# Performance work log

Hardware: AMD Instinct MI355X
Metric: run time of the kernel (lower is better)

Reference implementation:

```python
import jax, jax.numpy as jnp
import numpy as np

B, N, D, F = 16, 64, 32, 32  # batch, nodes, node_dim, nb_features


def setup_inputs() -> dict:
    key = jax.random.key(0)
    k1, k2, k3, k4, k5 = jax.random.split(key, 5)
    nodes = jax.random.normal(k1, (B, N, D), dtype=jnp.float32)
    edges = jax.random.normal(k2, (B, N * N, F), dtype=jnp.float32)
    mask = jax.random.randint(k3, (B, N * N, 1), 0, 2).astype(jnp.float32)
    # Linear(nb_features -> node_dim**2) params, torch-style fan-in scaling
    lim = 1.0 / np.sqrt(F)
    W = jax.random.uniform(k4, (D * D, F), dtype=jnp.float32, minval=-lim, maxval=lim)
    b = jax.random.uniform(k5, (D * D,), dtype=jnp.float32, minval=-lim, maxval=lim)
    return {"nodes": nodes, "edges": edges, "mask": mask, "W": W, "b": b}


def reference(nodes, edges, mask, W, b):
    Bn, Nn, d = nodes.shape
    # ECC weight generation: per-edge d x d matrix from edge features
    A = jax.nn.relu(jnp.einsum('bef,gf->beg', edges, W) + b)      # [B, N*N, d*d]
    A = A.reshape(Bn, Nn, Nn, d, d)                               # [B, i, j, d, d]
    # node_j tiling: flat edge index i*N+j pairs with source node j
    messages = jnp.einsum('bijde,bje->bijd', A, nodes)            # [B, i, j, d]
    masked = messages * mask.reshape(Bn, Nn, Nn, 1)
    agg_m = jnp.sum(masked, axis=2)                               # [B, N, d]
    return agg_m
```

## Files before the change

kernel.cpp:

```cpp
#include <hip/hip_runtime.h>
#include <hip/hip_bf16.h>


#define B_ 16
#define N_ 64
#define D_ 32
#define F_ 32
#define NP 33

typedef __attribute__((ext_vector_type(8))) short bf16x8;
typedef __attribute__((ext_vector_type(4))) float f32x4;

__device__ __forceinline__ short f2bf(float x) {
    unsigned u = __builtin_bit_cast(unsigned, x);
    u += 0x7fffu + ((u >> 16) & 1u);
    return (short)(u >> 16);
}

__global__ __launch_bounds__(256, 4) void ecc_fused_kernel(
    const float* __restrict__ nodes,
    const float* __restrict__ edges,
    const float* __restrict__ mask,
    const float* __restrict__ W,
    const float* __restrict__ bias,
    float* __restrict__ out)
{
    __shared__ float nmask[N_ * NP];

    const int tid  = threadIdx.x;
    const int lane = tid & 63;
    const int wv   = tid >> 6;
    const int col  = lane & 15;
    const int grp  = lane >> 4;
    const int bi   = blockIdx.x;
    const int b    = bi >> 6;
    const int i    = bi & 63;
    const int f0   = grp * 8;

    {
        const int j  = tid >> 2;
        const int c0 = (tid & 3) * 8;
        const float mk = mask[b * (N_ * N_) + i * N_ + j];
        const float* np = nodes + (b * N_ + j) * D_ + c0;
        f32x4 v0 = *(const f32x4*)np;
        f32x4 v1 = *(const f32x4*)(np + 4);
        float* dst = &nmask[j * NP + c0];
        dst[0] = v0[0] * mk; dst[1] = v0[1] * mk;
        dst[2] = v0[2] * mk; dst[3] = v0[3] * mk;
        dst[4] = v1[0] * mk; dst[5] = v1[1] * mk;
        dst[6] = v1[2] * mk; dst[7] = v1[3] * mk;
    }
    __syncthreads();

    const float* eb = edges + (b * (N_ * N_) + i * N_) * F_;
    bf16x8 bfrag[4];
#pragma unroll
    for (int jt = 0; jt < 4; ++jt) {
        const float* s = eb + (jt * 16 + col) * F_ + f0;
        f32x4 e0 = *(const f32x4*)s;
        f32x4 e1 = *(const f32x4*)(s + 4);
        bf16x8 t;
        t[0] = f2bf(e0[0]); t[1] = f2bf(e0[1]); t[2] = f2bf(e0[2]); t[3] = f2bf(e0[3]);
        t[4] = f2bf(e1[0]); t[5] = f2bf(e1[1]); t[6] = f2bf(e1[2]); t[7] = f2bf(e1[3]);
        bfrag[jt] = t;
    }

    float acc[8] = {0.f, 0.f, 0.f, 0.f, 0.f, 0.f, 0.f, 0.f};

#pragma unroll 1
    for (int par = 0; par < 2; ++par) {
        float nd[4][4];
#pragma unroll
        for (int jt = 0; jt < 4; ++jt) {
            const float* n = &nmask[(jt * 16 + col) * NP + par * 16 + grp * 4];
            nd[jt][0] = n[0]; nd[jt][1] = n[1];
            nd[jt][2] = n[2]; nd[jt][3] = n[3];
        }
#pragma unroll
        for (int g8 = 0; g8 < 8; ++g8) {
            const int gt = wv * 16 + g8 * 2 + par;
            const float* ws = W + (gt * 16 + col) * F_ + f0;
            f32x4 w0 = *(const f32x4*)ws;
            f32x4 w1 = *(const f32x4*)(ws + 4);
            bf16x8 afrag;
            afrag[0] = f2bf(w0[0]); afrag[1] = f2bf(w0[1]);
            afrag[2] = f2bf(w0[2]); afrag[3] = f2bf(w0[3]);
            afrag[4] = f2bf(w1[0]); afrag[5] = f2bf(w1[1]);
            afrag[6] = f2bf(w1[2]); afrag[7] = f2bf(w1[3]);

            f32x4 bfr = *(const f32x4*)(bias + gt * 16 + grp * 4);

#pragma unroll
            for (int jt = 0; jt < 4; ++jt) {
                f32x4 c = __builtin_amdgcn_mfma_f32_16x16x32_bf16(afrag, bfrag[jt], bfr, 0, 0, 0);
                float s = fmaxf(c[0], 0.f) * nd[jt][0];
                s += fmaxf(c[1], 0.f) * nd[jt][1];
                s += fmaxf(c[2], 0.f) * nd[jt][2];
                s += fmaxf(c[3], 0.f) * nd[jt][3];
                acc[g8] += s;
            }
        }
    }

#pragma unroll
    for (int dl = 0; dl < 8; ++dl) {
        float v = acc[dl];
#pragma unroll
        for (int off = 32; off > 0; off >>= 1) v += __shfl_xor(v, off, 64);
        acc[dl] = v;
    }

    if (lane == 0) {
        float* op = out + (b * N_ + i) * D_ + wv * 8;
#pragma unroll
        for (int dl = 0; dl < 8; ++dl) op[dl] = acc[dl];
    }
}

extern "C" void kernel_launch(void* const* d_in, const int* in_sizes, int n_in,
                              void* d_out, int out_size, void* d_ws, size_t ws_size,
                              hipStream_t stream) {
    const float* nodes = (const float*)d_in[0];
    const float* edges = (const float*)d_in[1];
    const float* mask  = (const float*)d_in[2];
    const float* W     = (const float*)d_in[3];
    const float* bias  = (const float*)d_in[4];
    float* outp        = (float*)d_out;

    ecc_fused_kernel<<<dim3(B_ * N_), dim3(256), 0, stream>>>(
        nodes, edges, mask, W, bias, outp);
}
```

Before: 105.1 us.

## Stage bf16-converted W half and bias in LDS per parity pass

```diff
diff --git a/kernel.cpp b/kernel.cpp
--- a/kernel.cpp
+++ b/kernel.cpp
@@ -17,7 +17,7 @@
     return (short)(u >> 16);
 }
 
-__global__ __launch_bounds__(256, 4) void ecc_fused_kernel(
+__global__ __launch_bounds__(256) void ecc_fused_kernel(
     const float* __restrict__ nodes,
     const float* __restrict__ edges,
     const float* __restrict__ mask,
@@ -25,7 +25,9 @@
     const float* __restrict__ bias,
     float* __restrict__ out)
 {
+    __shared__ short wlds[512 * F_];
     __shared__ float nmask[N_ * NP];
+    __shared__ float blds[D_ * D_];
 
     const int tid  = threadIdx.x;
     const int lane = tid & 63;
@@ -49,8 +51,8 @@
         dst[2] = v0[2] * mk; dst[3] = v0[3] * mk;
         dst[4] = v1[0] * mk; dst[5] = v1[1] * mk;
         dst[6] = v1[2] * mk; dst[7] = v1[3] * mk;
+        *(f32x4*)(blds + tid * 4) = *(const f32x4*)(bias + tid * 4);
     }
-    __syncthreads();
 
     const float* eb = edges + (b * (N_ * N_) + i * N_) * F_;
     bf16x8 bfrag[4];
@@ -69,6 +71,26 @@
 
 #pragma unroll 1
     for (int par = 0; par < 2; ++par) {
+        __syncthreads();
+
+#pragma unroll 2
+        for (int k = 0; k < 8; ++k) {
+            const int lidx = k * 2048 + tid * 8;
+            const int lr   = lidx >> 5;
+            const int fo   = lidx & 31;
+            const int g    = (((lr >> 4) * 2 + par) * 16) + (lr & 15);
+            const float* s = W + g * F_ + fo;
+            f32x4 a0 = *(const f32x4*)s;
+            f32x4 a1 = *(const f32x4*)(s + 4);
+            bf16x8 t;
+            t[0] = f2bf(a0[0]); t[1] = f2bf(a0[1]);
+            t[2] = f2bf(a0[2]); t[3] = f2bf(a0[3]);
+            t[4] = f2bf(a1[0]); t[5] = f2bf(a1[1]);
+            t[6] = f2bf(a1[2]); t[7] = f2bf(a1[3]);
+            *(bf16x8*)(wlds + lidx) = t;
+        }
+        __syncthreads();
+
         float nd[4][4];
 #pragma unroll
         for (int jt = 0; jt < 4; ++jt) {
@@ -76,19 +98,13 @@
             nd[jt][0] = n[0]; nd[jt][1] = n[1];
             nd[jt][2] = n[2]; nd[jt][3] = n[3];
         }
-#pragma unroll
+
+#pragma unroll 1
         for (int g8 = 0; g8 < 8; ++g8) {
-            const int gt = wv * 16 + g8 * 2 + par;
-            const float* ws = W + (gt * 16 + col) * F_ + f0;
-            f32x4 w0 = *(const f32x4*)ws;
-            f32x4 w1 = *(const f32x4*)(ws + 4);
-            bf16x8 afrag;
-            afrag[0] = f2bf(w0[0]); afrag[1] = f2bf(w0[1]);
-            afrag[2] = f2bf(w0[2]); afrag[3] = f2bf(w0[3]);
-            afrag[4] = f2bf(w1[0]); afrag[5] = f2bf(w1[1]);
-            afrag[6] = f2bf(w1[2]); afrag[7] = f2bf(w1[3]);
-
-            f32x4 bfr = *(const f32x4*)(bias + gt * 16 + grp * 4);
+            const int gt   = wv * 16 + g8 * 2 + par;
+            const int lrow = (wv * 8 + g8) * 16 + col;
+            bf16x8 afrag = *(const bf16x8*)(wlds + lrow * F_ + f0);
+            f32x4 bfr = *(const f32x4*)(blds + gt * 16 + grp * 4);
 
 #pragma unroll
             for (int jt = 0; jt < 4; ++jt) {
```

Result: faster. 86.75 us (-17.5%).
